# Kernel optimization log

Measured on AMD Instinct MI355X. Metric: run time of the kernel, lower is better.

## Reference

```python
import jax, jax.numpy as jnp
import numpy as np

B, S, D, H = 2, 2048, 1024, 16
HD = D // H  # head_dim = 64

def setup_inputs() -> dict:
    key = jax.random.key(0)
    ks = jax.random.split(key, 5)
    scale = 0.02
    return {
        "x":  jax.random.normal(ks[0], (B, S, D), dtype=jnp.float32),
        "Wq": jax.random.normal(ks[1], (D, D), dtype=jnp.float32) * scale,
        "Wk": jax.random.normal(ks[2], (D, D), dtype=jnp.float32) * scale,
        "Wv": jax.random.normal(ks[3], (D, D), dtype=jnp.float32) * scale,
        "Wo": jax.random.normal(ks[4], (D, D), dtype=jnp.float32) * scale,
    }

def reference(x, Wq, Wk, Wv, Wo):
    b, s, d = x.shape
    # projections (bias-free linear): [b,s,d] @ [d,d]
    q = (x @ Wq).reshape(b, s, H, HD).transpose(0, 2, 1, 3)  # [b,h,s,hd]
    k = (x @ Wk).reshape(b, s, H, HD).transpose(0, 2, 1, 3)
    v = (x @ Wv).reshape(b, s, H, HD).transpose(0, 2, 1, 3)
    scale = jnp.asarray(1.0 / np.sqrt(HD), dtype=x.dtype)
    scores = jnp.einsum('bhqd,bhkd->bhqk', q, k) * scale  # [b,h,s,s]
    causal = jnp.tril(jnp.ones((s, s), dtype=bool))
    scores = jnp.where(causal, scores, jnp.asarray(-jnp.inf, dtype=scores.dtype))
    attn = jax.nn.softmax(scores, axis=-1)
    out = jnp.einsum('bhqk,bhkd->bhqd', attn, v)  # [b,h,s,hd]
    out = out.transpose(0, 2, 1, 3).reshape(b, s, d)
    return out @ Wo
```

## Files before the change

### kernel.cpp

```cpp
#include <hip/hip_runtime.h>
#include <hip/hip_bf16.h>
#include <cstdint>

typedef __bf16 bf16;
typedef bf16 bf16x4v __attribute__((ext_vector_type(4)));
typedef bf16 bf16x8 __attribute__((ext_vector_type(8)));
typedef float f32x4 __attribute__((ext_vector_type(4)));

#define MFMA16(a, b, c) __builtin_amdgcn_mfma_f32_16x16x32_bf16(a, b, c, 0, 0, 0)

struct rawF { f32x4 a, b; };
__device__ inline rawF ldr(const float* p) {
  rawF r; r.a = *(const f32x4*)p; r.b = *(const f32x4*)(p + 4); return r;
}
__device__ inline bf16x8 ldr(const bf16* p) { return *(const bf16x8*)p; }
__device__ inline bf16x8 cv(const rawF& r) {
  bf16x8 o;
#pragma unroll
  for (int i = 0; i < 4; ++i) { o[i] = (bf16)r.a[i]; o[i + 4] = (bf16)r.b[i]; }
  return o;
}
__device__ inline bf16x8 cv(const bf16x8& r) { return r; }
__device__ inline void stC(bf16* C, size_t i, float v) { C[i] = (bf16)v; }
__device__ inline void stC(float* C, size_t i, float v) { C[i] = v; }

__global__ __launch_bounds__(256) void prep_wt(const float* __restrict__ W0,
                                               const float* __restrict__ W1,
                                               const float* __restrict__ W2,
                                               bf16* __restrict__ Wt, int n) {
  const float* Ws[3] = {W0, W1, W2};
  const float* W = Ws[blockIdx.z];
  bf16* out = Wt + (size_t)blockIdx.z * n * n;
  __shared__ bf16 t[32][33];
  int bx = blockIdx.x * 32, by = blockIdx.y * 32;
  int tx = threadIdx.x & 31, ty = threadIdx.x >> 5;
#pragma unroll
  for (int i = 0; i < 32; i += 8)
    t[ty + i][tx] = (bf16)W[(size_t)(by + ty + i) * n + bx + tx];
  __syncthreads();
#pragma unroll
  for (int i = 0; i < 32; i += 8)
    out[(size_t)(bx + ty + i) * n + by + tx] = t[tx][ty + i];
}

__global__ __launch_bounds__(256) void vtrans(const bf16* __restrict__ V, bf16* __restrict__ Vt) {
  constexpr int Sn = 2048, Dn = 1024;
  __shared__ bf16 t[32][33];
  int s0 = blockIdx.x * 32, hd0 = blockIdx.y * 32, bh = blockIdx.z;
  int b = bh >> 4, h = bh & 15;
  int tx = threadIdx.x & 31, ty = threadIdx.x >> 5;
#pragma unroll
  for (int i = 0; i < 32; i += 8)
    t[ty + i][tx] = V[(size_t)(b * Sn + s0 + ty + i) * Dn + h * 64 + hd0 + tx];
  __syncthreads();
#pragma unroll
  for (int i = 0; i < 32; i += 8)
    Vt[(size_t)bh * 64 * Sn + (size_t)(hd0 + ty + i) * Sn + s0 + tx] = t[tx][ty + i];
}

template <typename TA, typename TC>
__global__ __launch_bounds__(256) void gemm_bt3(const TA* __restrict__ A,
                                                const bf16* __restrict__ Bt0,
                                                const bf16* __restrict__ Bt1,
                                                const bf16* __restrict__ Bt2,
                                                TC* __restrict__ C0, TC* __restrict__ C1,
                                                TC* __restrict__ C2, int M, int N, int K,
                                                int nblk) {
  constexpr int LDA = 40, LDB = 40;
  __shared__ bf16 As[128 * LDA];
  __shared__ bf16 Bs[128 * LDB];
  int tid = threadIdx.x, wave = tid >> 6, lane = tid & 63;
  int la = lane & 15, quad = lane >> 4;
  int wr = (wave >> 1) * 64, wc = (wave & 1) * 64;
  int by = blockIdx.y;
  int sel = by / nblk;
  int n0 = (by - sel * nblk) * 128;
  const bf16* Bm = sel == 0 ? Bt0 : (sel == 1 ? Bt1 : Bt2);
  TC* C = sel == 0 ? C0 : (sel == 1 ? C1 : C2);
  const TA* Ab = A + (size_t)blockIdx.x * 128 * K;

  int ar[2], ac[2];
#pragma unroll
  for (int p = 0; p < 2; ++p) {
    int li = (tid + p * 256) * 8;
    ar[p] = li >> 5; ac[p] = li & 31;
  }

  f32x4 zero = {0.f, 0.f, 0.f, 0.f};
  f32x4 acc[4][4];
#pragma unroll
  for (int i = 0; i < 4; ++i)
#pragma unroll
    for (int j = 0; j < 4; ++j) acc[i][j] = zero;

  decltype(ldr((const TA*)nullptr)) pa[2];
  bf16x8 pb[2];
#pragma unroll
  for (int p = 0; p < 2; ++p) {
    pa[p] = ldr(&Ab[(size_t)ar[p] * K + ac[p]]);
    pb[p] = ldr(&Bm[(size_t)(n0 + ar[p]) * K + ac[p]]);
  }

  for (int k0 = 0; k0 < K; k0 += 32) {
#pragma unroll
    for (int p = 0; p < 2; ++p) {
      *(bf16x8*)&As[ar[p] * LDA + ac[p]] = cv(pa[p]);
      *(bf16x8*)&Bs[ar[p] * LDB + ac[p]] = pb[p];
    }
    __syncthreads();
    int k1 = k0 + 32;
    if (k1 < K) {
#pragma unroll
      for (int p = 0; p < 2; ++p) {
        pa[p] = ldr(&Ab[(size_t)ar[p] * K + k1 + ac[p]]);
        pb[p] = ldr(&Bm[(size_t)(n0 + ar[p]) * K + k1 + ac[p]]);
      }
    }
    bf16x8 af[4], bfr[4];
#pragma unroll
    for (int i = 0; i < 4; ++i)
      af[i] = *(const bf16x8*)&As[(wr + i * 16 + la) * LDA + quad * 8];
#pragma unroll
    for (int j = 0; j < 4; ++j)
      bfr[j] = *(const bf16x8*)&Bs[(wc + j * 16 + la) * LDB + quad * 8];
#pragma unroll
    for (int i = 0; i < 4; ++i)
#pragma unroll
      for (int j = 0; j < 4; ++j) acc[i][j] = MFMA16(af[i], bfr[j], acc[i][j]);
    __syncthreads();
  }
#pragma unroll
  for (int i = 0; i < 4; ++i) {
#pragma unroll
    for (int j = 0; j < 4; ++j) {
      int col = n0 + wc + j * 16 + la;
#pragma unroll
      for (int r = 0; r < 4; ++r) {
        int row = blockIdx.x * 128 + wr + i * 16 + quad * 4 + r;
        stC(C, (size_t)row * N + col, acc[i][j][r]);
      }
    }
  }
}

__device__ __forceinline__ void seg_step(const bf16* __restrict__ Ksb,
                                         const bf16* __restrict__ Vsb,
                                         bf16* __restrict__ Psw, const bf16x8* aq,
                                         f32x4* o, float& m_l, float& l_l,
                                         int la, int quad, int kb, int q0, bool diag) {
  const int LDK = 72, LDP = 72;
  const float MASK = -3.0e4f;
  f32x4 zero = {0.f, 0.f, 0.f, 0.f};
  f32x4 s[4];
#pragma unroll
  for (int nt = 0; nt < 4; ++nt) {
    bf16x8 k0f = *(const bf16x8*)&Ksb[(nt * 16 + la) * LDK + quad * 8];
    bf16x8 k1f = *(const bf16x8*)&Ksb[(nt * 16 + la) * LDK + 32 + quad * 8];
    f32x4 z = zero;
    z = MFMA16(k0f, aq[0], z);
    z = MFMA16(k1f, aq[1], z);
    s[nt] = z;
  }
  if (diag) {
    int qa = q0 + la;
#pragma unroll
    for (int nt = 0; nt < 4; ++nt)
#pragma unroll
      for (int r = 0; r < 4; ++r) {
        int ka = kb + nt * 16 + quad * 4 + r;
        s[nt][r] = (ka > qa) ? MASK : s[nt][r];
      }
  }
  float mx = m_l;
#pragma unroll
  for (int nt = 0; nt < 4; ++nt)
#pragma unroll
    for (int r = 0; r < 4; ++r) mx = fmaxf(mx, s[nt][r]);
  mx = fmaxf(mx, __shfl_xor(mx, 16, 64));
  mx = fmaxf(mx, __shfl_xor(mx, 32, 64));
  float alpha = exp2f(m_l - mx);
  float rs = 0.f;
#pragma unroll
  for (int nt = 0; nt < 4; ++nt)
#pragma unroll
    for (int r = 0; r < 4; ++r) {
      float p = exp2f(s[nt][r] - mx);
      s[nt][r] = p;
      rs += p;
    }
  rs += __shfl_xor(rs, 16, 64);
  rs += __shfl_xor(rs, 32, 64);
  l_l = l_l * alpha + rs;
  m_l = mx;
#pragma unroll
  for (int nt = 0; nt < 4; ++nt) {
    bf16x4v pk;
#pragma unroll
    for (int r = 0; r < 4; ++r) pk[r] = (bf16)s[nt][r];
    *(bf16x4v*)&Psw[la * LDP + nt * 16 + quad * 4] = pk;
  }
  float ab[4];
#pragma unroll
  for (int r = 0; r < 4; ++r) ab[r] = __shfl(alpha, quad * 4 + r, 64);
#pragma unroll
  for (int nt = 0; nt < 4; ++nt)
#pragma unroll
    for (int r = 0; r < 4; ++r) o[nt][r] *= ab[r];
#pragma unroll
  for (int kc = 0; kc < 2; ++kc) {
    bf16x8 ap = *(const bf16x8*)&Psw[la * LDP + kc * 32 + quad * 8];
#pragma unroll
    for (int nt = 0; nt < 4; ++nt) {
      bf16x8 bv = *(const bf16x8*)&Vsb[(nt * 16 + la) * LDK + kc * 32 + quad * 8];
      o[nt] = MFMA16(ap, bv, o[nt]);
    }
  }
}

__global__ __launch_bounds__(256) void flash_attn(const bf16* __restrict__ Q,
                                                  const bf16* __restrict__ Kg,
                                                  const bf16* __restrict__ Vtg,
                                                  bf16* __restrict__ O) {
  constexpr int D = 1024, S = 2048;
  const int LDK = 72;
  const float MASK = -3.0e4f;
  const float SCL2 = 0.18033688011112042f;
  __shared__ bf16 Ks[2][64 * 72];
  __shared__ bf16 Vs[2][64 * 72];
  __shared__ bf16 Ps[4][16 * 72];

  int bx = blockIdx.x, by = blockIdx.y;
  int p = (by & 16) ? (15 - bx) : bx;
  int qtA = 31 - p, qtB = p;
  int b = by >> 4, h = by & 15;
  int tid = threadIdx.x, wave = tid >> 6, lane = tid & 63;
  int la = lane & 15, quad = lane >> 4;
  int q0A = qtA * 64 + wave * 16, q0B = qtB * 64 + wave * 16;
  const size_t base = (size_t)b * S * D + (size_t)h * 64;
  const bf16* Qg = Q + base;
  const bf16* Kb = Kg + base;
  const bf16* Vb = Vtg + (size_t)by * 64 * S;
  int r0 = tid >> 3, c0 = (tid & 7) * 8;

  bf16x8 aqA[2], aqB[2];
#pragma unroll
  for (int kc = 0; kc < 2; ++kc) {
    bf16x8 ta = *(const bf16x8*)&Qg[(size_t)(q0A + la) * D + kc * 32 + quad * 8];
    bf16x8 tb = *(const bf16x8*)&Qg[(size_t)(q0B + la) * D + kc * 32 + quad * 8];
#pragma unroll
    for (int i = 0; i < 8; ++i) {
      ta[i] = (bf16)((float)ta[i] * SCL2);
      tb[i] = (bf16)((float)tb[i] * SCL2);
    }
    aqA[kc] = ta; aqB[kc] = tb;
  }

  f32x4 zero = {0.f, 0.f, 0.f, 0.f};
  f32x4 oA[4], oB[4];
  float mA = MASK, lA = 0.f, mB = MASK, lB = 0.f;
#pragma unroll
  for (int nt = 0; nt < 4; ++nt) { oA[nt] = zero; oB[nt] = zero; }

  bf16x8 kr0 = *(const bf16x8*)&Kb[(size_t)r0 * D + c0];
  bf16x8 kr1 = *(const bf16x8*)&Kb[(size_t)(r0 + 32) * D + c0];
  bf16x8 vr0 = *(const bf16x8*)&Vb[(size_t)r0 * S + c0];
  bf16x8 vr1 = *(const bf16x8*)&Vb[(size_t)(r0 + 32) * S + c0];
  *(bf16x8*)&Ks[0][r0 * LDK + c0] = kr0;
  *(bf16x8*)&Ks[0][(r0 + 32) * LDK + c0] = kr1;
  *(bf16x8*)&Vs[0][r0 * LDK + c0] = vr0;
  *(bf16x8*)&Vs[0][(r0 + 32) * LDK + c0] = vr1;
  __syncthreads();

  int ntA = qtA + 1;
  for (int t = 0; t < ntA; ++t) {
    int kb = t * 64;
    int cur = t & 1, nxt = cur ^ 1;
    bool more = (t + 1 < ntA);
    if (more) {
      int kb2 = kb + 64;
      kr0 = *(const bf16x8*)&Kb[(size_t)(kb2 + r0) * D + c0];
      kr1 = *(const bf16x8*)&Kb[(size_t)(kb2 + r0 + 32) * D + c0];
      vr0 = *(const bf16x8*)&Vb[(size_t)r0 * S + kb2 + c0];
      vr1 = *(const bf16x8*)&Vb[(size_t)(r0 + 32) * S + kb2 + c0];
    }
    seg_step(Ks[cur], Vs[cur], Ps[wave], aqA, oA, mA, lA, la, quad, kb, q0A, t == qtA);
    if (t <= qtB)
      seg_step(Ks[cur], Vs[cur], Ps[wave], aqB, oB, mB, lB, la, quad, kb, q0B, t == qtB);
    if (more) {
      *(bf16x8*)&Ks[nxt][r0 * LDK + c0] = kr0;
      *(bf16x8*)&Ks[nxt][(r0 + 32) * LDK + c0] = kr1;
      *(bf16x8*)&Vs[nxt][r0 * LDK + c0] = vr0;
      *(bf16x8*)&Vs[nxt][(r0 + 32) * LDK + c0] = vr1;
      __syncthreads();
    }
  }

#pragma unroll
  for (int seg = 0; seg < 2; ++seg) {
    f32x4* o = seg == 0 ? oA : oB;
    float l_l = seg == 0 ? lA : lB;
    int q0 = seg == 0 ? q0A : q0B;
    float inv[4];
#pragma unroll
    for (int r = 0; r < 4; ++r) {
      float lv = __shfl(l_l, quad * 4 + r, 64);
      inv[r] = (lv > 1e-30f) ? 1.0f / lv : 0.0f;
    }
#pragma unroll
    for (int nt = 0; nt < 4; ++nt) {
      int hd = nt * 16 + la;
#pragma unroll
      for (int r = 0; r < 4; ++r) {
        int row = q0 + quad * 4 + r;
        O[base + (size_t)row * D + hd] = (bf16)(o[nt][r] * inv[r]);
      }
    }
  }
}

extern "C" void kernel_launch(void* const* d_in, const int* in_sizes, int n_in,
                              void* d_out, int out_size, void* d_ws, size_t ws_size,
                              hipStream_t stream) {
  constexpr int B = 2, S = 2048, D = 1024;
  constexpr int M = B * S;
  constexpr size_t WN = (size_t)D * D;
  constexpr size_t XN = (size_t)M * D;

  const float* x = (const float*)d_in[0];
  const float* Wq = (const float*)d_in[1];
  const float* Wk = (const float*)d_in[2];
  const float* Wv = (const float*)d_in[3];
  const float* Wo = (const float*)d_in[4];
  float* out = (float*)d_out;

  if (ws_size < 2 * XN * sizeof(bf16)) return;
  bf16* Qb = (bf16*)d_ws;
  bf16* R2 = Qb + XN;
  bf16* Kb = (bf16*)d_out;
  bf16* Vb = Kb + XN;

  prep_wt<<<dim3(32, 32, 3), 256, 0, stream>>>(Wq, Wk, Wv, R2, D);
  gemm_bt3<float, bf16><<<dim3(M / 128, 24), 256, 0, stream>>>(
      x, R2, R2 + WN, R2 + 2 * WN, Qb, Kb, Vb, M, D, D, 8);
  vtrans<<<dim3(S / 32, 2, 32), 256, 0, stream>>>(Vb, R2);
  flash_attn<<<dim3(16, 32), 256, 0, stream>>>(Qb, Kb, R2, Qb);
  prep_wt<<<dim3(32, 32, 1), 256, 0, stream>>>(Wo, Wo, Wo, R2, D);
  gemm_bt3<bf16, float><<<dim3(M / 128, 8), 256, 0, stream>>>(
      Qb, R2, R2, R2, out, out, out, M, D, D, 8);
}
```

Baseline: 196.6 us.

## Load GEMM B (and bf16 A) tiles directly into LDS with swizzled layout

Replaces the register-staged prefetch of the bf16 weight tile (and the A tile when A is bf16) with global_load_lds direct-to-LDS transfers. The LDS layout becomes a rotated, swizzled 16-row block layout so the MFMA fragment reads avoid bank conflicts without padding. This removes the register round trip and the separate LDS store. It also drops the register double-buffered prefetch for those operands, so global latency is no longer hidden behind compute and is now exposed at each barrier.

```diff
diff --git a/kernel.cpp b/kernel.cpp
--- a/kernel.cpp
+++ b/kernel.cpp
@@ -1,6 +1,7 @@
 #include <hip/hip_runtime.h>
 #include <hip/hip_bf16.h>
 #include <cstdint>
+#include <type_traits>
 
 typedef __bf16 bf16;
 typedef bf16 bf16x4v __attribute__((ext_vector_type(4)));
@@ -13,16 +14,19 @@
 __device__ inline rawF ldr(const float* p) {
   rawF r; r.a = *(const f32x4*)p; r.b = *(const f32x4*)(p + 4); return r;
 }
-__device__ inline bf16x8 ldr(const bf16* p) { return *(const bf16x8*)p; }
 __device__ inline bf16x8 cv(const rawF& r) {
   bf16x8 o;
 #pragma unroll
   for (int i = 0; i < 4; ++i) { o[i] = (bf16)r.a[i]; o[i + 4] = (bf16)r.b[i]; }
   return o;
 }
-__device__ inline bf16x8 cv(const bf16x8& r) { return r; }
 __device__ inline void stC(bf16* C, size_t i, float v) { C[i] = (bf16)v; }
 __device__ inline void stC(float* C, size_t i, float v) { C[i] = v; }
+
+__device__ __forceinline__ void gload16(const bf16* g, bf16* l) {
+  __builtin_amdgcn_global_load_lds((const __attribute__((address_space(1))) void*)g,
+                                   (__attribute__((address_space(3))) void*)l, 16, 0, 0);
+}
 
 __global__ __launch_bounds__(256) void prep_wt(const float* __restrict__ W0,
                                                const float* __restrict__ W1,
@@ -66,9 +70,10 @@
                                                 TC* __restrict__ C0, TC* __restrict__ C1,
                                                 TC* __restrict__ C2, int M, int N, int K,
                                                 int nblk) {
-  constexpr int LDA = 40, LDB = 40;
-  __shared__ bf16 As[128 * LDA];
-  __shared__ bf16 Bs[128 * LDB];
+  constexpr bool AA = std::is_same<TA, bf16>::value;
+  constexpr int LDA = 40;
+  __shared__ alignas(16) bf16 As[AA ? 128 * 32 : 128 * LDA];
+  __shared__ alignas(16) bf16 Bs[128 * 32];
   int tid = threadIdx.x, wave = tid >> 6, lane = tid & 63;
   int la = lane & 15, quad = lane >> 4;
   int wr = (wave >> 1) * 64, wc = (wave & 1) * 64;
@@ -79,6 +84,14 @@
   TC* C = sel == 0 ? C0 : (sel == 1 ? C1 : C2);
   const TA* Ab = A + (size_t)blockIdx.x * 128 * K;
 
+  int sc = lane >> 4;
+  int sr = ((lane & 15) + 12 * sc) & 15;
+  const bf16* gB0 = &Bm[(size_t)(n0 + wave * 16 + sr) * K + 8 * sc];
+  const bf16* gB1 = &Bm[(size_t)(n0 + (wave + 4) * 16 + sr) * K + 8 * sc];
+  bf16* lB0 = &Bs[wave * 512];
+  bf16* lB1 = &Bs[(wave + 4) * 512];
+  int lam8 = 128 * quad + 8 * ((la + 4 * quad) & 15);
+
   int ar[2], ac[2];
 #pragma unroll
   for (int p = 0; p < 2; ++p) {
@@ -93,36 +106,43 @@
 #pragma unroll
     for (int j = 0; j < 4; ++j) acc[i][j] = zero;
 
-  decltype(ldr((const TA*)nullptr)) pa[2];
-  bf16x8 pb[2];
-#pragma unroll
-  for (int p = 0; p < 2; ++p) {
-    pa[p] = ldr(&Ab[(size_t)ar[p] * K + ac[p]]);
-    pb[p] = ldr(&Bm[(size_t)(n0 + ar[p]) * K + ac[p]]);
+  rawF pa[2];
+  if constexpr (!AA) {
+#pragma unroll
+    for (int p = 0; p < 2; ++p) pa[p] = ldr((const float*)&Ab[(size_t)ar[p] * K + ac[p]]);
   }
 
   for (int k0 = 0; k0 < K; k0 += 32) {
-#pragma unroll
-    for (int p = 0; p < 2; ++p) {
-      *(bf16x8*)&As[ar[p] * LDA + ac[p]] = cv(pa[p]);
-      *(bf16x8*)&Bs[ar[p] * LDB + ac[p]] = pb[p];
-    }
+    if constexpr (AA) {
+      gload16((const bf16*)&Ab[(size_t)(wave * 16 + sr) * K + k0 + 8 * sc], &As[wave * 512]);
+      gload16((const bf16*)&Ab[(size_t)((wave + 4) * 16 + sr) * K + k0 + 8 * sc],
+              &As[(wave + 4) * 512]);
+    } else {
+#pragma unroll
+      for (int p = 0; p < 2; ++p) *(bf16x8*)&As[ar[p] * LDA + ac[p]] = cv(pa[p]);
+    }
+    gload16(gB0 + k0, lB0);
+    gload16(gB1 + k0, lB1);
     __syncthreads();
-    int k1 = k0 + 32;
-    if (k1 < K) {
-#pragma unroll
-      for (int p = 0; p < 2; ++p) {
-        pa[p] = ldr(&Ab[(size_t)ar[p] * K + k1 + ac[p]]);
-        pb[p] = ldr(&Bm[(size_t)(n0 + ar[p]) * K + k1 + ac[p]]);
+    if constexpr (!AA) {
+      int k1 = k0 + 32;
+      if (k1 < K) {
+#pragma unroll
+        for (int p = 0; p < 2; ++p)
+          pa[p] = ldr((const float*)&Ab[(size_t)ar[p] * K + k1 + ac[p]]);
       }
     }
     bf16x8 af[4], bfr[4];
 #pragma unroll
-    for (int i = 0; i < 4; ++i)
-      af[i] = *(const bf16x8*)&As[(wr + i * 16 + la) * LDA + quad * 8];
+    for (int i = 0; i < 4; ++i) {
+      if constexpr (AA)
+        af[i] = *(const bf16x8*)&As[((wr >> 4) + i) * 512 + lam8];
+      else
+        af[i] = *(const bf16x8*)&As[(wr + i * 16 + la) * LDA + quad * 8];
+    }
 #pragma unroll
     for (int j = 0; j < 4; ++j)
-      bfr[j] = *(const bf16x8*)&Bs[(wc + j * 16 + la) * LDB + quad * 8];
+      bfr[j] = *(const bf16x8*)&Bs[((wc >> 4) + j) * 512 + lam8];
 #pragma unroll
     for (int i = 0; i < 4; ++i)
 #pragma unroll
```

Result: slower. 226.2 us (+15.0%).
